# Kernel optimization log

Hardware: AMD Instinct MI355X
Metric: run time of the kernel (lower is better)

## Reference

```python
import jax, jax.numpy as jnp
import numpy as np

TAU = 2.0
V_TH = 1.0
SG_ALPHA = 4.0  # spikingjelly surrogate.Sigmoid default

@jax.custom_vjp
def spike_fn(u):
    # heaviside(u) with sigmoid surrogate gradient; u = v - v_threshold
    return (u >= 0.0).astype(u.dtype)

def _spike_fwd(u):
    return spike_fn(u), u

def _spike_bwd(u, g):
    s = jax.nn.sigmoid(SG_ALPHA * u)
    return (g * SG_ALPHA * s * (1.0 - s),)

spike_fn.defvjp(_spike_fwd, _spike_bwd)

def lif_scan(h):
    # h: [T, B, D] input currents; multi-step LIF with hard reset to 0,
    # decay_input=True: v = v + (h - v) / tau
    def step(v, h_t):
        v = v + (h_t - v) / TAU
        s = spike_fn(v - V_TH)
        v = v * (1.0 - jax.lax.stop_gradient(s))  # detach_reset=True, v_reset=0
        return v, s
    v0 = jnp.zeros_like(h[0])
    _, spikes = jax.lax.scan(step, v0, h)
    return spikes  # [T, B, D]

def setup_inputs() -> dict:
    key = jax.random.key(0)
    k_x, k_w1, k_b1, k_w2, k_b2 = jax.random.split(key, 5)
    T, B, D, C = 32, 512, 1024, 1000
    lim1 = 1.0 / np.sqrt(D)
    return {
        "x": jax.random.normal(k_x, (T, B, D), dtype=jnp.float32),
        "W1": jax.random.uniform(k_w1, (D, D), jnp.float32, -lim1, lim1),
        "b1": jax.random.uniform(k_b1, (D,), jnp.float32, -lim1, lim1),
        "W2": jax.random.uniform(k_w2, (C, D), jnp.float32, -lim1, lim1),
        "b2": jax.random.uniform(k_b2, (C,), jnp.float32, -lim1, lim1),
    }

def reference(x, W1, b1, W2, b2):
    # linear_1: [T,B,D] @ [D,D]^T + b1
    h = jnp.einsum('tbd,ed->tbe', x, W1) + b1
    s = lif_scan(h)                               # [T,B,D] spikes in {0,1}
    y = jnp.einsum('tbd,cd->tbc', s, W2) + b2     # [T,B,C]
    y = y.mean(axis=0)                            # [B,C]
    return jax.nn.log_softmax(y, axis=1)
```

## Files before the change

kernel.cpp:

```cpp
#include <hip/hip_runtime.h>
#include <math.h>

#define T_STEPS 32
#define B_SZ    512
#define D_SZ    1024
#define C_SZ    1000
#define KZ      8
#define HP      132

typedef __bf16 bf16x8 __attribute__((ext_vector_type(8)));
typedef float  f32x4  __attribute__((ext_vector_type(4)));

__device__ __forceinline__ unsigned short f2bf(float f) {
    unsigned u = __float_as_uint(f);
    unsigned r = u + 0x7FFFu + ((u >> 16) & 1u);
    return (unsigned short)(r >> 16);
}
__device__ __forceinline__ float bf2f(unsigned short b) {
    return __uint_as_float(((unsigned)b) << 16);
}

__device__ __forceinline__ void async_copy16(const void* g, void* l) {
    __builtin_amdgcn_global_load_lds(
        (const __attribute__((address_space(1))) unsigned int*)g,
        (__attribute__((address_space(3))) unsigned int*)l,
        16, 0, 0);
}

__device__ __forceinline__ bf16x8 cvt8(const float4 u, const float4 v) {
    bf16x8 r;
    r[0] = (__bf16)u.x; r[1] = (__bf16)u.y; r[2] = (__bf16)u.z; r[3] = (__bf16)u.w;
    r[4] = (__bf16)v.x; r[5] = (__bf16)v.y; r[6] = (__bf16)v.z; r[7] = (__bf16)v.w;
    return r;
}

#define NW14  262144
#define NW24  256000
#define NWTOT (NW14 + NW24)

__global__ __launch_bounds__(256) void cast_w_k(
    const float* __restrict__ W1, unsigned short* __restrict__ W1_bf,
    const float* __restrict__ W2, unsigned short* __restrict__ W2_bf)
{
    const int idx = blockIdx.x * 256 + threadIdx.x;
    const float4* s; ushort4* d; int j;
    if (idx < NW14) { s = (const float4*)W1; d = (ushort4*)W1_bf; j = idx; }
    else            { s = (const float4*)W2; d = (ushort4*)W2_bf; j = idx - NW14; }
    const float4 v = s[j];
    ushort4 o;
    o.x = f2bf(v.x); o.y = f2bf(v.y); o.z = f2bf(v.z); o.w = f2bf(v.w);
    d[j] = o;
}

__global__ __launch_bounds__(256) void gemm1_scan_k(
    const float* __restrict__ X, const unsigned short* __restrict__ Bm,
    const float* __restrict__ bias, unsigned short* __restrict__ cnt)
{
    __shared__ __align__(16) unsigned short smem[32768];

    const int tid  = threadIdx.x;
    const int wave = tid >> 6;
    const int lane = tid & 63;
    const int lm   = lane & 15;
    const int quad = lane >> 4;
    const int wm   = (wave >> 1) * 64;
    const int wn   = (wave & 1) * 64;

    const int f  = blockIdx.x;
    const int rr = f >> 9;
    const int cc = f & 7;
    const int ss = (f >> 3) & 63;
    const int xb = ss & 7;
    const int yb = rr * 64 + (ss >> 3) * 8 + cc;
    const int b0 = yb * 4;
    const int n0 = xb * 128;

    f32x4 acc[4][4];
    #pragma unroll
    for (int i = 0; i < 4; ++i)
        #pragma unroll
        for (int j = 0; j < 4; ++j)
            acc[i][j] = (f32x4){0.f, 0.f, 0.f, 0.f};

    int srow[4], sgq[4];
    size_t arowoff[4];
    unsigned ldsoffB[4];
    #pragma unroll
    for (int p = 0; p < 4; ++p) {
        const int s = p * 256 + tid;
        const int rho = s >> 3;
        srow[p] = rho;
        sgq[p]  = (s & 7) ^ (rho & 7);
        arowoff[p] = (size_t)((rho >> 2) * 512 + b0 + (rho & 3)) * D_SZ;
        ldsoffB[p] = (unsigned)(p * 256 + wave * 64) * 16u;
    }
    const int fq0 = quad ^ (lm & 7);

    float4 au[4], av[4];

#define LOAD_A(k0_) do {                                                        \
        _Pragma("unroll")                                                       \
        for (int p = 0; p < 4; ++p) {                                           \
            const float* srcp = X + arowoff[p] + (k0_) + sgq[p] * 8;            \
            au[p] = *(const float4*)(srcp);                                     \
            av[p] = *(const float4*)(srcp + 4);                                 \
        }                                                                       \
    } while (0)

#define STAGE_B(buf_, k0_) do {                                                 \
        char* bdst = (char*)(smem + 16384 + (buf_) * 8192);                     \
        _Pragma("unroll")                                                       \
        for (int p = 0; p < 4; ++p)                                             \
            async_copy16(Bm + (size_t)(n0 + srow[p]) * D_SZ + (k0_) + sgq[p] * 8,\
                         bdst + ldsoffB[p]);                                    \
    } while (0)

#define WRITE_A(buf_) do {                                                      \
        bf16x8* adst = (bf16x8*)(smem + (buf_) * 8192);                         \
        _Pragma("unroll")                                                       \
        for (int p = 0; p < 4; ++p)                                             \
            adst[p * 256 + tid] = cvt8(au[p], av[p]);                           \
    } while (0)

#define COMPUTE(buf_) do {                                                      \
        const bf16x8* Ar = (const bf16x8*)(smem + (buf_) * 8192);               \
        const bf16x8* Br = (const bf16x8*)(smem + 16384 + (buf_) * 8192);       \
        __builtin_amdgcn_s_setprio(1);                                          \
        _Pragma("unroll")                                                       \
        for (int kk = 0; kk < 2; ++kk) {                                        \
            const int fqk = fq0 ^ (kk * 4);                                     \
            bf16x8 af[4], bfr[4];                                               \
            _Pragma("unroll")                                                   \
            for (int i2 = 0; i2 < 4; ++i2) {                                    \
                af[i2]  = Ar[(wm + i2 * 16 + lm) * 8 + fqk];                    \
                bfr[i2] = Br[(wn + i2 * 16 + lm) * 8 + fqk];                    \
            }                                                                   \
            _Pragma("unroll")                                                   \
            for (int mi = 0; mi < 4; ++mi)                                      \
                _Pragma("unroll")                                               \
                for (int ni = 0; ni < 4; ++ni)                                  \
                    acc[mi][ni] = __builtin_amdgcn_mfma_f32_16x16x32_bf16(      \
                        af[mi], bfr[ni], acc[mi][ni], 0, 0, 0);                 \
        }                                                                       \
        __builtin_amdgcn_s_setprio(0);                                          \
    } while (0)

    LOAD_A(0);
    STAGE_B(0, 0);
    WRITE_A(0);
    __syncthreads();
    LOAD_A(64);
    STAGE_B(1, 64);

    for (int i = 0; i < 14; i += 2) {
        COMPUTE(0);
        WRITE_A(1);
        __syncthreads();
        LOAD_A((i + 2) * 64);
        STAGE_B(0, (i + 2) * 64);

        COMPUTE(1);
        WRITE_A(0);
        __syncthreads();
        LOAD_A((i + 3) * 64);
        STAGE_B(1, (i + 3) * 64);
    }
    COMPUTE(0);
    WRITE_A(1);
    __syncthreads();
    COMPUTE(1);
    __syncthreads();

#undef LOAD_A
#undef STAGE_B
#undef WRITE_A
#undef COMPUTE

    #pragma unroll
    for (int ni = 0; ni < 4; ++ni) {
        const int nn = wn + ni * 16 + lm;
        const float bv = bias[n0 + nn];
        #pragma unroll
        for (int mi = 0; mi < 4; ++mi) {
            const f32x4 v = acc[mi][ni];
            #pragma unroll
            for (int r = 0; r < 4; ++r)
                smem[(wm + mi * 16 + quad * 4 + r) * HP + nn] = f2bf(v[r] + bv);
        }
    }
    __syncthreads();

    {
        const unsigned* smemU = (const unsigned*)smem;
        const int bb = tid >> 6;
        const int c2 = tid & 63;
        float v0 = 0.f, cv0 = 0.f, v1 = 0.f, cv1 = 0.f;
        #pragma unroll
        for (int t = 0; t < T_STEPS; ++t) {
            const unsigned u = smemU[(t * 4 + bb) * (HP / 2) + c2];
            const float h0 = bf2f((unsigned short)(u & 0xFFFFu));
            const float h1 = bf2f((unsigned short)(u >> 16));
            v0 = 0.5f * (v0 + h0);
            const float s0 = (v0 >= 1.0f) ? 1.0f : 0.0f;
            cv0 += s0; v0 *= (1.0f - s0);
            v1 = 0.5f * (v1 + h1);
            const float s1 = (v1 >= 1.0f) ? 1.0f : 0.0f;
            cv1 += s1; v1 *= (1.0f - s1);
        }
        ushort2 o;
        o.x = f2bf(cv0); o.y = f2bf(cv1);
        *(ushort2*)&cnt[(size_t)(b0 + bb) * D_SZ + n0 + 2 * c2] = o;
    }
}

__global__ __launch_bounds__(256) void gemm2_splitk_k(
    const unsigned short* __restrict__ A, const unsigned short* __restrict__ Bm,
    float* __restrict__ partial)
{
    __shared__ __align__(16) unsigned short As[128 * 32];
    __shared__ __align__(16) unsigned short Bs[128 * 32];

    const int tid  = threadIdx.x;
    const int wave = tid >> 6;
    const int lane = tid & 63;
    const int lm   = lane & 15;
    const int quad = lane >> 4;
    const int wm   = (wave >> 1) * 64;
    const int wn   = (wave & 1) * 64;
    const int n0   = blockIdx.x * 128;
    const int m0   = blockIdx.y * 128;
    const int kz   = blockIdx.z;

    f32x4 acc[4][4];
    #pragma unroll
    for (int i = 0; i < 4; ++i)
        #pragma unroll
        for (int j = 0; j < 4; ++j)
            acc[i][j] = (f32x4){0.f, 0.f, 0.f, 0.f};

    int srow[2], sgq[2];
    unsigned ldsoff[2];
    #pragma unroll
    for (int p = 0; p < 2; ++p) {
        const int s = p * 256 + tid;
        srow[p] = s >> 2;
        sgq[p]  = (s & 3) ^ ((srow[p] >> 1) & 3);
        ldsoff[p] = (unsigned)(p * 256 + wave * 64) * 16u;
    }
    const int fq = quad ^ ((lm >> 1) & 3);

    const int kbeg = kz * (D_SZ / KZ);
    for (int k0 = kbeg; k0 < kbeg + D_SZ / KZ; k0 += 32) {
        #pragma unroll
        for (int p = 0; p < 2; ++p) {
            async_copy16(A + (size_t)(m0 + srow[p]) * D_SZ + k0 + sgq[p] * 8,
                         (char*)As + ldsoff[p]);
            int brow = n0 + srow[p];
            if (brow > C_SZ - 1) brow = C_SZ - 1;
            async_copy16(Bm + (size_t)brow * D_SZ + k0 + sgq[p] * 8,
                         (char*)Bs + ldsoff[p]);
        }
        __syncthreads();

        bf16x8 af[4], bfr[4];
        #pragma unroll
        for (int i = 0; i < 4; ++i) {
            af[i]  = ((const bf16x8*)As)[(wm + i * 16 + lm) * 4 + fq];
            bfr[i] = ((const bf16x8*)Bs)[(wn + i * 16 + lm) * 4 + fq];
        }
        #pragma unroll
        for (int mi = 0; mi < 4; ++mi)
            #pragma unroll
            for (int ni = 0; ni < 4; ++ni)
                acc[mi][ni] = __builtin_amdgcn_mfma_f32_16x16x32_bf16(
                    af[mi], bfr[ni], acc[mi][ni], 0, 0, 0);
        __syncthreads();
    }

    #pragma unroll
    for (int ni = 0; ni < 4; ++ni) {
        const int nn = n0 + wn + ni * 16 + lm;
        if (nn >= C_SZ) continue;
        #pragma unroll
        for (int mi = 0; mi < 4; ++mi) {
            const f32x4 v = acc[mi][ni];
            #pragma unroll
            for (int r = 0; r < 4; ++r) {
                const int mm = m0 + wm + mi * 16 + quad * 4 + r;
                partial[((size_t)kz * B_SZ + mm) * C_SZ + nn] = v[r];
            }
        }
    }
}

__global__ __launch_bounds__(256) void reduce_lsm_k(
    const float* __restrict__ partial, const float* __restrict__ b2,
    float* __restrict__ out)
{
    __shared__ float red_max[4];
    __shared__ float red_sum[4];

    const int b   = blockIdx.x;
    const int tid = threadIdx.x;

    float vals[4];
    float m = -1e30f;
    #pragma unroll
    for (int k = 0; k < 4; ++k) {
        const int c = tid + k * 256;
        if (c < C_SZ) {
            float s = 0.f;
            #pragma unroll
            for (int z = 0; z < KZ; ++z)
                s += partial[((size_t)z * B_SZ + b) * C_SZ + c];
            vals[k] = s * (1.0f / (float)T_STEPS) + b2[c];
        } else {
            vals[k] = -1e30f;
        }
        m = fmaxf(m, vals[k]);
    }
    #pragma unroll
    for (int off = 32; off > 0; off >>= 1)
        m = fmaxf(m, __shfl_down(m, off, 64));
    const int wave = tid >> 6;
    const int lane = tid & 63;
    if (lane == 0) red_max[wave] = m;
    __syncthreads();
    m = fmaxf(fmaxf(red_max[0], red_max[1]), fmaxf(red_max[2], red_max[3]));

    float s = 0.f;
    #pragma unroll
    for (int k = 0; k < 4; ++k) {
        const int c = tid + k * 256;
        if (c < C_SZ) s += __expf(vals[k] - m);
    }
    #pragma unroll
    for (int off = 32; off > 0; off >>= 1)
        s += __shfl_down(s, off, 64);
    if (lane == 0) red_sum[wave] = s;
    __syncthreads();
    s = red_sum[0] + red_sum[1] + red_sum[2] + red_sum[3];

    const float lse = m + logf(s);
    #pragma unroll
    for (int k = 0; k < 4; ++k) {
        const int c = tid + k * 256;
        if (c < C_SZ) out[(size_t)b * C_SZ + c] = vals[k] - lse;
    }
}

extern "C" void kernel_launch(void* const* d_in, const int* in_sizes, int n_in,
                              void* d_out, int out_size, void* d_ws, size_t ws_size,
                              hipStream_t stream)
{
    const float* x  = (const float*)d_in[0];
    const float* W1 = (const float*)d_in[1];
    const float* b1 = (const float*)d_in[2];
    const float* W2 = (const float*)d_in[3];
    const float* b2 = (const float*)d_in[4];
    float* out = (float*)d_out;

    char* ws = (char*)d_ws;
    unsigned short* W1_bf   = (unsigned short*)(ws);
    unsigned short* W2_bf   = (unsigned short*)(ws + 2097152);
    unsigned short* cnt_bf  = (unsigned short*)(ws + 4145152);
    float*          partial = (float*)(ws + 5193728);

    cast_w_k<<<NWTOT / 256, 256, 0, stream>>>(W1, W1_bf, W2, W2_bf);

    gemm1_scan_k<<<(B_SZ / 4) * (D_SZ / 128), 256, 0, stream>>>(
        x, W1_bf, b1, cnt_bf);

    {
        dim3 grid((C_SZ + 127) / 128, B_SZ / 128, KZ);
        gemm2_splitk_k<<<grid, 256, 0, stream>>>(cnt_bf, W2_bf, partial);
    }

    reduce_lsm_k<<<B_SZ, 256, 0, stream>>>(partial, b2, out);
}
```

Baseline: 168.8 us.

## Pre-cast X to bf16 and stream it via async LDS copies in GEMM1

Adds a combined cast kernel that converts X along with both weight matrices to bf16 in workspace. GEMM1 then loads bf16 X tiles with async global-to-LDS copies instead of loading fp32 and converting in-kernel. This simplifies the GEMM1 pipeline but adds an extra full pass over X: 64MB read plus 32MB written. The new path runs only when the workspace is large enough, with the old path kept as a fallback.

```diff
diff --git a/kernel.cpp b/kernel.cpp
--- a/kernel.cpp
+++ b/kernel.cpp
@@ -34,9 +34,27 @@
     return r;
 }
 
+#define NX4   4194304
 #define NW14  262144
 #define NW24  256000
 #define NWTOT (NW14 + NW24)
+#define NCTOT (NX4 + NW14 + NW24)
+
+__global__ __launch_bounds__(256) void cast_all_k(
+    const float* __restrict__ X,  unsigned short* __restrict__ X_bf,
+    const float* __restrict__ W1, unsigned short* __restrict__ W1_bf,
+    const float* __restrict__ W2, unsigned short* __restrict__ W2_bf)
+{
+    const int idx = blockIdx.x * 256 + threadIdx.x;
+    const float4* s; ushort4* d; int j;
+    if (idx < NX4)              { s = (const float4*)X;  d = (ushort4*)X_bf;  j = idx; }
+    else if (idx < NX4 + NW14)  { s = (const float4*)W1; d = (ushort4*)W1_bf; j = idx - NX4; }
+    else                        { s = (const float4*)W2; d = (ushort4*)W2_bf; j = idx - NX4 - NW14; }
+    const float4 v = s[j];
+    ushort4 o;
+    o.x = f2bf(v.x); o.y = f2bf(v.y); o.z = f2bf(v.z); o.w = f2bf(v.w);
+    d[j] = o;
+}
 
 __global__ __launch_bounds__(256) void cast_w_k(
     const float* __restrict__ W1, unsigned short* __restrict__ W1_bf,
@@ -52,7 +70,144 @@
     d[j] = o;
 }
 
-__global__ __launch_bounds__(256) void gemm1_scan_k(
+__global__ __launch_bounds__(256) void gemm1_scan_bf_k(
+    const unsigned short* __restrict__ Xb, const unsigned short* __restrict__ Bm,
+    const float* __restrict__ bias, unsigned short* __restrict__ cnt)
+{
+    __shared__ __align__(16) unsigned short smem[32768];
+
+    const int tid  = threadIdx.x;
+    const int wave = tid >> 6;
+    const int lane = tid & 63;
+    const int lm   = lane & 15;
+    const int quad = lane >> 4;
+    const int wm   = (wave >> 1) * 64;
+    const int wn   = (wave & 1) * 64;
+
+    const int f  = blockIdx.x;
+    const int rr = f >> 9;
+    const int cc = f & 7;
+    const int ss = (f >> 3) & 63;
+    const int xb = ss & 7;
+    const int yb = rr * 64 + (ss >> 3) * 8 + cc;
+    const int b0 = yb * 4;
+    const int n0 = xb * 128;
+
+    f32x4 acc[4][4];
+    #pragma unroll
+    for (int i = 0; i < 4; ++i)
+        #pragma unroll
+        for (int j = 0; j < 4; ++j)
+            acc[i][j] = (f32x4){0.f, 0.f, 0.f, 0.f};
+
+    int srow[4], sgq[4];
+    size_t aoff[4];
+    unsigned ldsoff[4];
+    #pragma unroll
+    for (int p = 0; p < 4; ++p) {
+        const int s = p * 256 + tid;
+        const int rho = s >> 3;
+        srow[p] = rho;
+        sgq[p]  = (s & 7) ^ (rho & 7);
+        aoff[p] = (size_t)((rho >> 2) * 512 + b0 + (rho & 3)) * D_SZ;
+        ldsoff[p] = (unsigned)(p * 256 + wave * 64) * 16u;
+    }
+    const int fq0 = quad ^ (lm & 7);
+
+#define STAGE(buf_, k0_) do {                                                    \
+        char* abase = (char*)smem + (buf_) * 16384;                              \
+        char* bbase = (char*)smem + 32768 + (buf_) * 16384;                      \
+        _Pragma("unroll")                                                        \
+        for (int p = 0; p < 4; ++p)                                              \
+            async_copy16(Xb + aoff[p] + (k0_) + sgq[p] * 8,                      \
+                         abase + ldsoff[p]);                                     \
+        _Pragma("unroll")                                                        \
+        for (int p = 0; p < 4; ++p)                                              \
+            async_copy16(Bm + (size_t)(n0 + srow[p]) * D_SZ + (k0_) + sgq[p] * 8,\
+                         bbase + ldsoff[p]);                                     \
+    } while (0)
+
+#define COMPUTE(buf_) do {                                                       \
+        const bf16x8* Ar = (const bf16x8*)((char*)smem + (buf_) * 16384);        \
+        const bf16x8* Br = (const bf16x8*)((char*)smem + 32768 + (buf_) * 16384);\
+        __builtin_amdgcn_s_setprio(1);                                           \
+        _Pragma("unroll")                                                        \
+        for (int kk = 0; kk < 2; ++kk) {                                         \
+            const int fqk = fq0 ^ (kk * 4);                                      \
+            bf16x8 af[4], bfr[4];                                                \
+            _Pragma("unroll")                                                    \
+            for (int i2 = 0; i2 < 4; ++i2) {                                     \
+                af[i2]  = Ar[(wm + i2 * 16 + lm) * 8 + fqk];                     \
+                bfr[i2] = Br[(wn + i2 * 16 + lm) * 8 + fqk];                     \
+            }                                                                    \
+            _Pragma("unroll")                                                    \
+            for (int mi = 0; mi < 4; ++mi)                                       \
+                _Pragma("unroll")                                                \
+                for (int ni = 0; ni < 4; ++ni)                                   \
+                    acc[mi][ni] = __builtin_amdgcn_mfma_f32_16x16x32_bf16(       \
+                        af[mi], bfr[ni], acc[mi][ni], 0, 0, 0);                  \
+        }                                                                        \
+        __builtin_amdgcn_s_setprio(0);                                           \
+    } while (0)
+
+    STAGE(0, 0);
+    __syncthreads();
+
+    for (int t = 0; t < 14; t += 2) {
+        STAGE(1, (t + 1) * 64);
+        COMPUTE(0);
+        __syncthreads();
+        STAGE(0, (t + 2) * 64);
+        COMPUTE(1);
+        __syncthreads();
+    }
+    STAGE(1, 15 * 64);
+    COMPUTE(0);
+    __syncthreads();
+    COMPUTE(1);
+    __syncthreads();
+
+#undef STAGE
+#undef COMPUTE
+
+    #pragma unroll
+    for (int ni = 0; ni < 4; ++ni) {
+        const int nn = wn + ni * 16 + lm;
+        const float bv = bias[n0 + nn];
+        #pragma unroll
+        for (int mi = 0; mi < 4; ++mi) {
+            const f32x4 v = acc[mi][ni];
+            #pragma unroll
+            for (int r = 0; r < 4; ++r)
+                smem[(wm + mi * 16 + quad * 4 + r) * HP + nn] = f2bf(v[r] + bv);
+        }
+    }
+    __syncthreads();
+
+    {
+        const unsigned* smemU = (const unsigned*)smem;
+        const int bb = tid >> 6;
+        const int c2 = tid & 63;
+        float v0 = 0.f, cv0 = 0.f, v1 = 0.f, cv1 = 0.f;
+        #pragma unroll
+        for (int t = 0; t < T_STEPS; ++t) {
+            const unsigned u = smemU[(t * 4 + bb) * (HP / 2) + c2];
+            const float h0 = bf2f((unsigned short)(u & 0xFFFFu));
+            const float h1 = bf2f((unsigned short)(u >> 16));
+            v0 = 0.5f * (v0 + h0);
+            const float s0 = (v0 >= 1.0f) ? 1.0f : 0.0f;
+            cv0 += s0; v0 *= (1.0f - s0);
+            v1 = 0.5f * (v1 + h1);
+            const float s1 = (v1 >= 1.0f) ? 1.0f : 0.0f;
+            cv1 += s1; v1 *= (1.0f - s1);
+        }
+        ushort2 o;
+        o.x = f2bf(cv0); o.y = f2bf(cv1);
+        *(ushort2*)&cnt[(size_t)(b0 + bb) * D_SZ + n0 + 2 * c2] = o;
+    }
+}
+
+__global__ __launch_bounds__(256) void gemm1_scan_f32_k(
     const float* __restrict__ X, const unsigned short* __restrict__ Bm,
     const float* __restrict__ bias, unsigned short* __restrict__ cnt)
 {
@@ -361,20 +516,35 @@
     float* out = (float*)d_out;
 
     char* ws = (char*)d_ws;
-    unsigned short* W1_bf   = (unsigned short*)(ws);
-    unsigned short* W2_bf   = (unsigned short*)(ws + 2097152);
-    unsigned short* cnt_bf  = (unsigned short*)(ws + 4145152);
-    float*          partial = (float*)(ws + 5193728);
-
-    cast_w_k<<<NWTOT / 256, 256, 0, stream>>>(W1, W1_bf, W2, W2_bf);
-
-    gemm1_scan_k<<<(B_SZ / 4) * (D_SZ / 128), 256, 0, stream>>>(
-        x, W1_bf, b1, cnt_bf);
-
-    {
-        dim3 grid((C_SZ + 127) / 128, B_SZ / 128, KZ);
-        gemm2_splitk_k<<<grid, 256, 0, stream>>>(cnt_bf, W2_bf, partial);
-    }
-
-    reduce_lsm_k<<<B_SZ, 256, 0, stream>>>(partial, b2, out);
-}
+
+    if (ws_size >= 38748160u) {
+        unsigned short* X_bf    = (unsigned short*)(ws);
+        float*          partial = (float*)(ws);
+        unsigned short* W1_bf   = (unsigned short*)(ws + 33554432);
+        unsigned short* W2_bf   = (unsigned short*)(ws + 35651584);
+        unsigned short* cnt_bf  = (unsigned short*)(ws + 37699584);
+
+        cast_all_k<<<NCTOT / 256, 256, 0, stream>>>(x, X_bf, W1, W1_bf, W2, W2_bf);
+        gemm1_scan_bf_k<<<(B_SZ / 4) * (D_SZ / 128), 256, 0, stream>>>(
+            X_bf, W1_bf, b1, cnt_bf);
+        {
+            dim3 grid((C_SZ + 127) / 128, B_SZ / 128, KZ);
+            gemm2_splitk_k<<<grid, 256, 0, stream>>>(cnt_bf, W2_bf, partial);
+        }
+        reduce_lsm_k<<<B_SZ, 256, 0, stream>>>(partial, b2, out);
+    } else {
+        unsigned short* W1_bf   = (unsigned short*)(ws);
+        unsigned short* W2_bf   = (unsigned short*)(ws + 2097152);
+        unsigned short* cnt_bf  = (unsigned short*)(ws + 4145152);
+        float*          partial = (float*)(ws + 5193728);
+
+        cast_w_k<<<NWTOT / 256, 256, 0, stream>>>(W1, W1_bf, W2, W2_bf);
+        gemm1_scan_f32_k<<<(B_SZ / 4) * (D_SZ / 128), 256, 0, stream>>>(
+            x, W1_bf, b1, cnt_bf);
+        {
+            dim3 grid((C_SZ + 127) / 128, B_SZ / 128, KZ);
+            gemm2_splitk_k<<<grid, 256, 0, stream>>>(cnt_bf, W2_bf, partial);
+        }
+        reduce_lsm_k<<<B_SZ, 256, 0, stream>>>(partial, b2, out);
+    }
+}
```

New measurement: 160.6 us. -4.9%, faster.
